# Kernel optimization log

Hardware: AMD Instinct MI355X
Metric: run time of the kernel (lower is better)

Reference implementation:

```python
import jax, jax.numpy as jnp
import numpy as np
import math

NUM_HEADS = 16
HEAD_DIM = 64
EMBED = 1024
NUM_BUCKETS = 32
MAX_DISTANCE = 128


def _relative_position_bucket(relative_position, num_buckets=NUM_BUCKETS, max_distance=MAX_DISTANCE):
    # bidirectional T5 bucketing
    nb = num_buckets // 2
    relative_buckets = (relative_position > 0).astype(jnp.int32) * nb
    rp = jnp.abs(relative_position)
    max_exact = nb // 2
    is_small = rp < max_exact
    rp_safe = jnp.maximum(rp, 1)  # avoid log(0); masked by is_small anyway
    rp_large = max_exact + (
        jnp.log(rp_safe.astype(jnp.float32) / max_exact)
        / math.log(max_distance / max_exact)
        * (nb - max_exact)
    ).astype(jnp.int32)
    rp_large = jnp.minimum(rp_large, nb - 1)
    return relative_buckets + jnp.where(is_small, rp, rp_large)


def compute_bias(rel_emb, q_len, k_len):
    ctx = jnp.arange(q_len)[:, None]
    mem = jnp.arange(k_len)[None, :]
    buckets = _relative_position_bucket(mem - ctx)  # [q,k]
    values = rel_emb[buckets]                       # [q,k,H]
    return jnp.transpose(values, (2, 0, 1))[None]   # [1,H,q,k]


def setup_inputs() -> dict:
    key = jax.random.key(0)
    ks = jax.random.split(key, 6)
    std = 0.02
    B, S = 2, 2048
    inner = NUM_HEADS * HEAD_DIM
    return {
        "input_ids": jax.random.normal(ks[0], (B, S, EMBED), dtype=jnp.float32),
        "Wq": jax.random.normal(ks[1], (EMBED, inner), dtype=jnp.float32) * std,
        "Wk": jax.random.normal(ks[2], (EMBED, inner), dtype=jnp.float32) * std,
        "Wv": jax.random.normal(ks[3], (EMBED, inner), dtype=jnp.float32) * std,
        "Wo": jax.random.normal(ks[4], (inner, EMBED), dtype=jnp.float32) * std,
        "rel_emb": jax.random.normal(ks[5], (NUM_BUCKETS, NUM_HEADS), dtype=jnp.float32) * std,
    }


def reference(input_ids, Wq, Wk, Wv, Wo, rel_emb):
    B, S, _ = input_ids.shape
    H, D = NUM_HEADS, HEAD_DIM
    q = (input_ids @ Wq).reshape(B, S, H, D).transpose(0, 2, 1, 3)  # [B,H,S,D]
    k = (input_ids @ Wk).reshape(B, S, H, D).transpose(0, 2, 1, 3)
    v = (input_ids @ Wv).reshape(B, S, H, D).transpose(0, 2, 1, 3)
    scores = jnp.einsum("bhqd,bhkd->bhqk", q, k)  # no 1/sqrt(d) scaling (T5 style)
    position_bias = compute_bias(rel_emb, S, S)   # [1,H,S,S]
    scores = scores + position_bias
    attn = jax.nn.softmax(scores, axis=-1)
    out = jnp.einsum("bhqk,bhkd->bhqd", attn, v)
    out = out.transpose(0, 2, 1, 3).reshape(B, S, H * D)
    out = out @ Wo
    return out, position_bias
```

## Files before the change

kernel.cpp:

```cpp
#include <hip/hip_runtime.h>
#include <stdint.h>

#define S_LEN 2048
#define NH 16
#define EMB 1024
#define L2E 1.44269504f

typedef __attribute__((ext_vector_type(8))) short bf16x8;
typedef __attribute__((ext_vector_type(4))) float floatx4;
typedef const __attribute__((address_space(1))) unsigned int* gas_u32p;
typedef __attribute__((address_space(3))) unsigned int* las_u32p;

static __device__ __forceinline__ void gld_lds16(const void* g, void* l) {
  __builtin_amdgcn_global_load_lds((gas_u32p)g, (las_u32p)l, 16, 0, 0);
}

static __device__ __forceinline__ unsigned short f2bf(float f) {
  unsigned int u = __float_as_uint(f);
  unsigned int r = (u + 0x7FFFu + ((u >> 16) & 1u)) >> 16;
  return (unsigned short)r;
}
static __device__ __forceinline__ unsigned short f2bf_fast(float f) {
  return (unsigned short)((__float_as_uint(f) + 0x8000u) >> 16);
}

static __device__ __forceinline__ void bias_block(int bb, int tid,
                                                  const float* __restrict__ lut,
                                                  float* __restrict__ bias_out) {
#pragma unroll 4
  for (int e = 0; e < 256; e++) {
    int i = (bb << 16) + (e << 8) + tid;
    int h = i >> 20;
    int rem = i & 1048575;
    int q = rem >> 9;
    int k4 = (rem & 511) << 2;
    const float* lr = lut + h * 4096 + (k4 - q + 2048);
    floatx4 v = (floatx4){lr[0], lr[1], lr[2], lr[3]};
    __builtin_nontemporal_store(v, (floatx4*)&bias_out[(size_t)i * 4]);
  }
}

__global__ __launch_bounds__(256) void prep_kernel(const float* __restrict__ X,
                                                   const float* __restrict__ Wq,
                                                   const float* __restrict__ Wk,
                                                   const float* __restrict__ Wv,
                                                   const float* __restrict__ Wo,
                                                   const float* __restrict__ rel,
                                                   unsigned short* __restrict__ Xb,
                                                   unsigned short* __restrict__ WT,
                                                   float* __restrict__ lut) {
  __shared__ float tile[32][33];
  const int bid = blockIdx.x, tid = threadIdx.x;
  if (bid < 4096) {
    int i = bid * 256 + tid;
    float4 v = ((const float4*)X)[i];
    ushort4 o;
    o.x = f2bf(v.x); o.y = f2bf(v.y); o.z = f2bf(v.z); o.w = f2bf(v.w);
    ((ushort4*)Xb)[i] = o;
  } else if (bid < 8192) {
    int w = (bid - 4096) >> 10, t = (bid - 4096) & 1023;
    const float* in = (w == 0) ? Wq : (w == 1) ? Wk : (w == 2) ? Wv : Wo;
    unsigned short* o = WT + (size_t)w * 1048576;
    int bx = t & 31, by = t >> 5;
    int tx = tid & 31, ty = tid >> 5;
    int x = bx * 32 + tx, y0 = by * 32 + ty;
#pragma unroll
    for (int j = 0; j < 4; j++)
      tile[ty + 8 * j][tx] = in[(y0 + 8 * j) * EMB + x];
    __syncthreads();
    int x2 = by * 32 + tx, y2 = bx * 32 + ty;
#pragma unroll
    for (int j = 0; j < 4; j++)
      o[(y2 + 8 * j) * EMB + x2] = f2bf(tile[tx][ty + 8 * j]);
  } else {
    int idx = (bid - 8192) * 256 + tid;
    int delta = idx - 2048;
    int bucket = (delta > 0) ? 16 : 0;
    int rp = (delta < 0) ? -delta : delta;
    int bl;
    if (rp < 8) bl = rp;
    else bl = 8 + (rp >= 12) + (rp >= 16) + (rp >= 23) + (rp >= 32) + (rp >= 46) + (rp >= 64) + (rp >= 91);
    bucket += bl;
#pragma unroll
    for (int h = 0; h < NH; h++)
      lut[h * 4096 + idx] = rel[bucket * NH + h];
  }
}

__global__ __launch_bounds__(256) void gemm_qkv(const unsigned short* __restrict__ A,
                                                const unsigned short* __restrict__ BT,
                                                unsigned short* __restrict__ oQ,
                                                unsigned short* __restrict__ oK,
                                                unsigned short* __restrict__ oV,
                                                const float* __restrict__ lut,
                                                float* __restrict__ bias_out) {
  __shared__ __align__(16) unsigned short As[128 * 64];
  __shared__ __align__(16) unsigned short Bs[128 * 64];
  const int tid = threadIdx.x;
  const int id = blockIdx.x;
  if (id >= 768) {
    bias_block(id - 768, tid, lut, bias_out);
    return;
  }
  const int wave = tid >> 6, lane = tid & 63;
  const int quad = lane >> 4, lm = lane & 15;
  const int wm = wave & 1, wn = wave >> 1;
  const int mBase = (id / 24) * 128, nBase = (id % 24) * 128;
  const int gg = (lane & 7) ^ (lane >> 3);
  const int srow = lane >> 3;
  floatx4 acc[4][4];
#pragma unroll
  for (int i = 0; i < 4; i++)
#pragma unroll
    for (int j = 0; j < 4; j++) acc[i][j] = (floatx4){0.f, 0.f, 0.f, 0.f};

  for (int kt = 0; kt < 16; kt++) {
    int k0 = kt * 64;
    __syncthreads();
#pragma unroll
    for (int c = 0; c < 4; c++) {
      int chunk = wave * 4 + c;
      int row = chunk * 8 + srow;
      gld_lds16(&A[(size_t)(mBase + row) * 1024 + k0 + gg * 8], &As[chunk * 512]);
      gld_lds16(&BT[(size_t)(nBase + row) * 1024 + k0 + gg * 8], &Bs[chunk * 512]);
    }
    __syncthreads();
#pragma unroll
    for (int hh = 0; hh < 2; hh++) {
      bf16x8 af[4], bfr[4];
#pragma unroll
      for (int i = 0; i < 4; i++)
        af[i] = *(const bf16x8*)&As[(wm * 64 + i * 16 + lm) * 64 + (((hh << 2) + quad) ^ (lm & 7)) * 8];
#pragma unroll
      for (int j = 0; j < 4; j++)
        bfr[j] = *(const bf16x8*)&Bs[(wn * 64 + j * 16 + lm) * 64 + (((hh << 2) + quad) ^ (lm & 7)) * 8];
#pragma unroll
      for (int i = 0; i < 4; i++)
#pragma unroll
        for (int j = 0; j < 4; j++)
          acc[i][j] = __builtin_amdgcn_mfma_f32_16x16x32_bf16(af[i], bfr[j], acc[i][j], 0, 0, 0);
    }
  }
  const int which = nBase >> 10;
  if (which == 2) {
#pragma unroll
    for (int i = 0; i < 4; i++)
#pragma unroll
      for (int j = 0; j < 4; j++) {
        int hd = (nBase - 2048) + wn * 64 + j * 16 + lm;
        int h = hd >> 6, d = hd & 63;
        int m = mBase + wm * 64 + i * 16 + quad * 4;
        int b = m >> 11, s = m & 2047;
        union { unsigned short u[4]; uint2 v; } pk;
#pragma unroll
        for (int r = 0; r < 4; r++) pk.u[r] = f2bf(acc[i][j][r]);
        *(uint2*)&oV[(((size_t)(b * NH + h) * 64 + d) * S_LEN) + s] = pk.v;
      }
  } else {
#pragma unroll
    for (int i = 0; i < 4; i++)
#pragma unroll
      for (int j = 0; j < 4; j++)
#pragma unroll
        for (int r = 0; r < 4; r++) {
          int row = mBase + wm * 64 + i * 16 + quad * 4 + r;
          int col = nBase + wn * 64 + j * 16 + lm;
          int b = row >> 11, s = row & 2047;
          int cw = col & 1023;
          int h = cw >> 6, d = cw & 63;
          float v = acc[i][j][r];
          if (which == 0) v *= L2E;
          unsigned short sv = f2bf(v);
          if (which == 0) oQ[(((size_t)(b * NH + h) * S_LEN + s) * 64) + d] = sv;
          else            oK[(((size_t)(b * NH + h) * S_LEN + s) * 64) + d] = sv;
        }
  }
}

__global__ __launch_bounds__(256) void gemm_out(const unsigned short* __restrict__ A,
                                                const unsigned short* __restrict__ BT,
                                                float* __restrict__ oF,
                                                const float* __restrict__ lut,
                                                float* __restrict__ bias_out) {
  __shared__ __align__(16) unsigned short As[128 * 64];
  __shared__ __align__(16) unsigned short Bs[128 * 64];
  const int tid = threadIdx.x;
  const int id = blockIdx.x;
  if (id >= 256) {
    bias_block(160 + (id - 256), tid, lut, bias_out);
    return;
  }
  const int wave = tid >> 6, lane = tid & 63;
  const int quad = lane >> 4, lm = lane & 15;
  const int wm = wave & 1, wn = wave >> 1;
  const int mBase = (id >> 3) * 128, nBase = (id & 7) * 128;
  const int gg = (lane & 7) ^ (lane >> 3);
  const int srow = lane >> 3;
  floatx4 acc[4][4];
#pragma unroll
  for (int i = 0; i < 4; i++)
#pragma unroll
    for (int j = 0; j < 4; j++) acc[i][j] = (floatx4){0.f, 0.f, 0.f, 0.f};

  for (int kt = 0; kt < 16; kt++) {
    int k0 = kt * 64;
    __syncthreads();
#pragma unroll
    for (int c = 0; c < 4; c++) {
      int chunk = wave * 4 + c;
      int row = chunk * 8 + srow;
      gld_lds16(&A[(size_t)(mBase + row) * 1024 + k0 + gg * 8], &As[chunk * 512]);
      gld_lds16(&BT[(size_t)(nBase + row) * 1024 + k0 + gg * 8], &Bs[chunk * 512]);
    }
    __syncthreads();
#pragma unroll
    for (int hh = 0; hh < 2; hh++) {
      bf16x8 af[4], bfr[4];
#pragma unroll
      for (int i = 0; i < 4; i++)
        af[i] = *(const bf16x8*)&As[(wm * 64 + i * 16 + lm) * 64 + (((hh << 2) + quad) ^ (lm & 7)) * 8];
#pragma unroll
      for (int j = 0; j < 4; j++)
        bfr[j] = *(const bf16x8*)&Bs[(wn * 64 + j * 16 + lm) * 64 + (((hh << 2) + quad) ^ (lm & 7)) * 8];
#pragma unroll
      for (int i = 0; i < 4; i++)
#pragma unroll
        for (int j = 0; j < 4; j++)
          acc[i][j] = __builtin_amdgcn_mfma_f32_16x16x32_bf16(af[i], bfr[j], acc[i][j], 0, 0, 0);
    }
  }
#pragma unroll
  for (int i = 0; i < 4; i++)
#pragma unroll
    for (int j = 0; j < 4; j++)
#pragma unroll
      for (int r = 0; r < 4; r++) {
        int row = mBase + wm * 64 + i * 16 + quad * 4 + r;
        int col = nBase + wn * 64 + j * 16 + lm;
        oF[(size_t)row * 1024 + col] = acc[i][j][r];
      }
}

__global__ __launch_bounds__(512, 4) void attn_kernel(const unsigned short* __restrict__ Qb,
                                                      const unsigned short* __restrict__ Kb,
                                                      const unsigned short* __restrict__ Vtb,
                                                      const float* __restrict__ lut,
                                                      unsigned short* __restrict__ Ob) {
  __shared__ __align__(16) unsigned short Kl[2][2][2048];
  __shared__ __align__(16) unsigned short Vl[2][2][2048];
  __shared__ __align__(16) unsigned short Pl[8][16 * 40];
  __shared__ float lutS[512];
  const int tid = threadIdx.x;
  const int wave = tid >> 6, lane = tid & 63;
  const int quad = lane >> 4, lm = lane & 15;
  const int ws = wave & 3, half = wave >> 2;
  const int ii = blockIdx.x;
  const int bh = (ii & 7) * 4 + ((ii >> 3) & 3);
  const int qTile = (ii >> 5) * 128;
  const int b = bh >> 4, h = bh & 15;
  const unsigned short* Qp = Qb + (size_t)bh * S_LEN * 64;
  const unsigned short* Kp = Kb + (size_t)bh * S_LEN * 64;
  const unsigned short* Vp = Vtb + (size_t)bh * 64 * S_LEN;
  const float* lrow = lut + h * 4096;
  const float cneg = lrow[0] * L2E, cpos = lrow[4095] * L2E;
  const int srow = lane >> 3;
  const int gg = (lane & 7) ^ (srow & 7);
  const int vrow = lane >> 2;
  const int vgg = (lane & 3) ^ ((lane >> 3) & 3);
  const int qw = qTile + ws * 32;

  lutS[tid & 511] = lrow[2048 - 256 + (tid & 511)] * L2E;

  bf16x8 aq[2][2];
#pragma unroll
  for (int g = 0; g < 2; g++)
#pragma unroll
    for (int hh = 0; hh < 2; hh++)
      aq[g][hh] = *(const bf16x8*)&Qp[(qw + g * 16 + lm) * 64 + hh * 32 + quad * 8];

  floatx4 accO[2][4];
#pragma unroll
  for (int g = 0; g < 2; g++)
#pragma unroll
    for (int d = 0; d < 4; d++) accO[g][d] = (floatx4){0.f, 0.f, 0.f, 0.f};
  float lp[2] = {0.f, 0.f};

  unsigned short* Pw = Pl[wave];
  const int vswz = ((lm >> 1) & 3);

  {
    const int kBase = half << 10;
    gld_lds16(&Kp[(size_t)(kBase + ws * 8 + srow) * 64 + gg * 8], &Kl[half][0][ws * 512]);
    gld_lds16(&Vp[(size_t)(ws * 16 + vrow) * S_LEN + kBase + vgg * 8], &Vl[half][0][ws * 512]);
  }

  for (int ktl = 0; ktl < 32; ktl++) {
    const int buf = ktl & 1;
    const int kBase = (half << 10) + ktl * 32;
    __syncthreads();
    if (ktl < 31) {
      const int kn = kBase + 32;
      gld_lds16(&Kp[(size_t)(kn + ws * 8 + srow) * 64 + gg * 8], &Kl[half][buf ^ 1][ws * 512]);
      gld_lds16(&Vp[(size_t)(ws * 16 + vrow) * S_LEN + kn + vgg * 8], &Vl[half][buf ^ 1][ws * 512]);
    }
    const unsigned short* Kbuf = Kl[half][buf];
    const unsigned short* Vbuf = Vl[half][buf];

    const bool farTile = (kBase + 122 <= qTile) || (kBase >= qTile + 218);
    const float cfar = (kBase < qTile) ? cneg : cpos;

    floatx4 s4[2][2];
#pragma unroll
    for (int nt = 0; nt < 2; nt++) {
      int rbase = (nt * 16 + lm) * 64;
      bf16x8 kf0 = *(const bf16x8*)&Kbuf[rbase + ((quad ^ (lm & 7)) << 3)];
      bf16x8 kf1 = *(const bf16x8*)&Kbuf[rbase + (((4 + quad) ^ (lm & 7)) << 3)];
#pragma unroll
      for (int g = 0; g < 2; g++) {
        floatx4 z = (floatx4){0.f, 0.f, 0.f, 0.f};
        z = __builtin_amdgcn_mfma_f32_16x16x32_bf16(kf0, aq[g][0], z, 0, 0, 0);
        z = __builtin_amdgcn_mfma_f32_16x16x32_bf16(kf1, aq[g][1], z, 0, 0, 0);
        s4[g][nt] = z;
      }
    }

    bf16x8 pa[2];
#pragma unroll
    for (int g = 0; g < 2; g++) {
      const int b0 = kBase + quad * 4 - (qw + g * 16 + lm) + 256;
      float psum = 0.f;
#pragma unroll
      for (int nt = 0; nt < 2; nt++) {
        union { unsigned short u[4]; uint2 v; } pk;
#pragma unroll
        for (int r = 0; r < 4; r++) {
          float sv;
          if (farTile) sv = s4[g][nt][r] + cfar;
          else         sv = s4[g][nt][r] + lutS[b0 + nt * 16 + r];
          float p = __builtin_amdgcn_exp2f(sv);
          psum += p;
          pk.u[r] = f2bf_fast(p);
        }
        *(uint2*)&Pw[lm * 40 + nt * 16 + quad * 4] = pk.v;
      }
      lp[g] += psum;
      pa[g] = *(const bf16x8*)&Pw[lm * 40 + quad * 8];
    }

#pragma unroll
    for (int d = 0; d < 4; d++) {
      bf16x8 vf = *(const bf16x8*)&Vbuf[(d * 16 + lm) * 32 + ((quad ^ vswz) << 3)];
      accO[0][d] = __builtin_amdgcn_mfma_f32_16x16x32_bf16(pa[0], vf, accO[0][d], 0, 0, 0);
      accO[1][d] = __builtin_amdgcn_mfma_f32_16x16x32_bf16(pa[1], vf, accO[1][d], 0, 0, 0);
    }
  }

#pragma unroll
  for (int g = 0; g < 2; g++) {
    lp[g] += __shfl_xor(lp[g], 16, 64);
    lp[g] += __shfl_xor(lp[g], 32, 64);
  }

  __syncthreads();
  float* Ox = (ws < 2) ? ((float*)&Kl[0][0][0]) + ws * 2048 : ((float*)&Vl[0][0][0]) + (ws - 2) * 2048;
  float* lpf = (float*)&Pl[0][0];
  if (half == 1) {
#pragma unroll
    for (int g = 0; g < 2; g++) {
#pragma unroll
      for (int d = 0; d < 4; d++)
#pragma unroll
        for (int r = 0; r < 4; r++)
          Ox[(g * 16 + quad * 4 + r) * 64 + d * 16 + lm] = accO[g][d][r];
      if (quad == 0) lpf[ws * 32 + g * 16 + lm] = lp[g];
    }
  }
  __syncthreads();
  if (half == 0) {
    float ltot[2];
#pragma unroll
    for (int g = 0; g < 2; g++) ltot[g] = lp[g] + lpf[ws * 32 + g * 16 + lm];
#pragma unroll
    for (int g = 0; g < 2; g++) {
      float linv[4];
#pragma unroll
      for (int r = 0; r < 4; r++) linv[r] = 1.f / __shfl(ltot[g], quad * 4 + r, 64);
#pragma unroll
      for (int d = 0; d < 4; d++)
#pragma unroll
        for (int r = 0; r < 4; r++) {
          float val = accO[g][d][r] + Ox[(g * 16 + quad * 4 + r) * 64 + d * 16 + lm];
          int q = qw + g * 16 + quad * 4 + r;
          int col = h * 64 + d * 16 + lm;
          Ob[((size_t)(b * S_LEN + q)) * 1024 + col] = f2bf_fast(val * linv[r]);
        }
    }
  }
}

extern "C" void kernel_launch(void* const* d_in, const int* in_sizes, int n_in,
                              void* d_out, int out_size, void* d_ws, size_t ws_size,
                              hipStream_t stream) {
  const float* X   = (const float*)d_in[0];
  const float* Wq  = (const float*)d_in[1];
  const float* Wk  = (const float*)d_in[2];
  const float* Wv  = (const float*)d_in[3];
  const float* Wo  = (const float*)d_in[4];
  const float* rel = (const float*)d_in[5];
  float* out = (float*)d_out;
  float* bias_out = out + 4194304;

  char* ws = (char*)d_ws;
  unsigned short* Xb  = (unsigned short*)(ws);
  unsigned short* WT  = (unsigned short*)(ws + (size_t)(8u << 20));
  unsigned short* Qb  = (unsigned short*)(ws + (size_t)(16u << 20));
  unsigned short* Kb  = (unsigned short*)(ws + (size_t)(24u << 20));
  unsigned short* Vtb = (unsigned short*)(ws + (size_t)(32u << 20));
  unsigned short* Ob  = (unsigned short*)(ws + (size_t)(40u << 20));
  float* lut          = (float*)(ws + (size_t)(48u << 20));

  prep_kernel<<<8208, 256, 0, stream>>>(X, Wq, Wk, Wv, Wo, rel, Xb, WT, lut);
  gemm_qkv<<<928, 256, 0, stream>>>(Xb, WT, Qb, Kb, Vtb, lut, bias_out);
  attn_kernel<<<512, 512, 0, stream>>>(Qb, Kb, Vtb, lut, Ob);
  gemm_out<<<352, 256, 0, stream>>>(Ob, WT + 3 * 1048576, out, lut, bias_out);
}
```

Baseline: 411.6 us.

## Keep P in registers via permuted K rows and permlane32 swap instead of LDS

Permutes the K-row mapping in the QK^T MFMA so that the softmax probabilities land in a register layout that can be repacked into the PV MFMA A-operand with v_cvt_pk_bf16_f32 and v_permlane32_swap, removing the per-wave P round trip through shared memory. The P LDS buffer is deleted and lutS is reused for the partial row sums. It also raises wave priority around the MFMA blocks with s_setprio. The aim is to cut LDS traffic, LDS footprint and the write-to-read latency between the two matmuls. The risk is a wrong operand mapping, and reusing lutS for the row sums depends on the barrier ordering.

```diff
diff --git a/kernel.cpp b/kernel.cpp
--- a/kernel.cpp
+++ b/kernel.cpp
@@ -248,7 +248,6 @@
                                                       unsigned short* __restrict__ Ob) {
   __shared__ __align__(16) unsigned short Kl[2][2][2048];
   __shared__ __align__(16) unsigned short Vl[2][2][2048];
-  __shared__ __align__(16) unsigned short Pl[8][16 * 40];
   __shared__ float lutS[512];
   const int tid = threadIdx.x;
   const int wave = tid >> 6, lane = tid & 63;
@@ -268,6 +267,8 @@
   const int vrow = lane >> 2;
   const int vgg = (lane & 3) ^ ((lane >> 3) & 3);
   const int qw = qTile + ws * 32;
+  const int lmP = (lm & 3) | ((lm & 4) << 1) | ((lm & 8) >> 1);
+  const int qq4 = ((quad & 1) << 3) | ((quad & 2) << 1);
 
   lutS[tid & 511] = lrow[2048 - 256 + (tid & 511)] * L2E;
 
@@ -285,7 +286,6 @@
     for (int d = 0; d < 4; d++) accO[g][d] = (floatx4){0.f, 0.f, 0.f, 0.f};
   float lp[2] = {0.f, 0.f};
 
-  unsigned short* Pw = Pl[wave];
   const int vswz = ((lm >> 1) & 3);
 
   {
@@ -310,11 +310,12 @@
     const float cfar = (kBase < qTile) ? cneg : cpos;
 
     floatx4 s4[2][2];
+    __builtin_amdgcn_s_setprio(1);
 #pragma unroll
     for (int nt = 0; nt < 2; nt++) {
-      int rbase = (nt * 16 + lm) * 64;
-      bf16x8 kf0 = *(const bf16x8*)&Kbuf[rbase + ((quad ^ (lm & 7)) << 3)];
-      bf16x8 kf1 = *(const bf16x8*)&Kbuf[rbase + (((4 + quad) ^ (lm & 7)) << 3)];
+      int rbase = (nt * 16 + lmP) * 64;
+      bf16x8 kf0 = *(const bf16x8*)&Kbuf[rbase + ((quad ^ (lmP & 7)) << 3)];
+      bf16x8 kf1 = *(const bf16x8*)&Kbuf[rbase + (((4 + quad) ^ (lmP & 7)) << 3)];
 #pragma unroll
       for (int g = 0; g < 2; g++) {
         floatx4 z = (floatx4){0.f, 0.f, 0.f, 0.f};
@@ -323,36 +324,51 @@
         s4[g][nt] = z;
       }
     }
+    __builtin_amdgcn_s_setprio(0);
 
     bf16x8 pa[2];
 #pragma unroll
     for (int g = 0; g < 2; g++) {
-      const int b0 = kBase + quad * 4 - (qw + g * 16 + lm) + 256;
+      const int b0 = kBase + qq4 - (qw + g * 16 + lm) + 256;
       float psum = 0.f;
+      unsigned w00, w01, w10, w11;
 #pragma unroll
       for (int nt = 0; nt < 2; nt++) {
-        union { unsigned short u[4]; uint2 v; } pk;
-#pragma unroll
-        for (int r = 0; r < 4; r++) {
-          float sv;
-          if (farTile) sv = s4[g][nt][r] + cfar;
-          else         sv = s4[g][nt][r] + lutS[b0 + nt * 16 + r];
-          float p = __builtin_amdgcn_exp2f(sv);
-          psum += p;
-          pk.u[r] = f2bf_fast(p);
+        float sv0, sv1, sv2, sv3;
+        if (farTile) {
+          sv0 = s4[g][nt][0] + cfar; sv1 = s4[g][nt][1] + cfar;
+          sv2 = s4[g][nt][2] + cfar; sv3 = s4[g][nt][3] + cfar;
+        } else {
+          const float* lb = &lutS[b0 + nt * 16];
+          sv0 = s4[g][nt][0] + lb[0]; sv1 = s4[g][nt][1] + lb[1];
+          sv2 = s4[g][nt][2] + lb[2]; sv3 = s4[g][nt][3] + lb[3];
         }
-        *(uint2*)&Pw[lm * 40 + nt * 16 + quad * 4] = pk.v;
+        float p0 = __builtin_amdgcn_exp2f(sv0);
+        float p1 = __builtin_amdgcn_exp2f(sv1);
+        float p2 = __builtin_amdgcn_exp2f(sv2);
+        float p3 = __builtin_amdgcn_exp2f(sv3);
+        psum += (p0 + p1) + (p2 + p3);
+        unsigned wlo, whi;
+        asm("v_cvt_pk_bf16_f32 %0, %1, %2" : "=v"(wlo) : "v"(p0), "v"(p1));
+        asm("v_cvt_pk_bf16_f32 %0, %1, %2" : "=v"(whi) : "v"(p2), "v"(p3));
+        if (nt == 0) { w00 = wlo; w01 = whi; } else { w10 = wlo; w11 = whi; }
       }
       lp[g] += psum;
-      pa[g] = *(const bf16x8*)&Pw[lm * 40 + quad * 8];
-    }
-
+      asm("v_permlane32_swap_b32 %0, %1" : "+v"(w00), "+v"(w10));
+      asm("v_permlane32_swap_b32 %0, %1" : "+v"(w01), "+v"(w11));
+      union { unsigned u[4]; bf16x8 v; } pk;
+      pk.u[0] = w00; pk.u[1] = w01; pk.u[2] = w10; pk.u[3] = w11;
+      pa[g] = pk.v;
+    }
+
+    __builtin_amdgcn_s_setprio(1);
 #pragma unroll
     for (int d = 0; d < 4; d++) {
       bf16x8 vf = *(const bf16x8*)&Vbuf[(d * 16 + lm) * 32 + ((quad ^ vswz) << 3)];
       accO[0][d] = __builtin_amdgcn_mfma_f32_16x16x32_bf16(pa[0], vf, accO[0][d], 0, 0, 0);
       accO[1][d] = __builtin_amdgcn_mfma_f32_16x16x32_bf16(pa[1], vf, accO[1][d], 0, 0, 0);
     }
+    __builtin_amdgcn_s_setprio(0);
   }
 
 #pragma unroll
@@ -363,7 +379,7 @@
 
   __syncthreads();
   float* Ox = (ws < 2) ? ((float*)&Kl[0][0][0]) + ws * 2048 : ((float*)&Vl[0][0][0]) + (ws - 2) * 2048;
-  float* lpf = (float*)&Pl[0][0];
+  float* lpf = lutS;
   if (half == 1) {
 #pragma unroll
     for (int g = 0; g < 2; g++) {
```

Measured after the change: 401.1 us. 1.03x faster.
